# Kernel tuning notes

Measured on AMD Instinct MI355X. Metric: run time of the kernel, lower is better.

## Reference

```python
import jax, jax.numpy as jnp
import numpy as np

P_MINUS_1 = 1.0      # p=2 -> (p-1)
LCP_BETA = 32.0
LOG_ALPHA = float(np.log(2.0))  # alpha=2.0
KDIG = 8
N_HEAD = 16


def _rope(x, cos, sin):
    # x: (B,T,H,D), cos/sin: (T,D//2)
    d = x.shape[-1] // 2
    x1, x2 = x[..., :d], x[..., d:]
    c = cos[None, :, None, :]
    s = sin[None, :, None, :]
    return jnp.concatenate([x1 * c - x2 * s, x1 * s + x2 * c], axis=-1)


def _rms_norm(x, eps=1e-6):
    return x * jax.lax.rsqrt(jnp.mean(jnp.square(x), axis=-1, keepdims=True) + eps)


def setup_inputs() -> dict:
    key = jax.random.key(0)
    ks = jax.random.split(key, 9)
    B, T, C, H = 2, 512, 1024, N_HEAD
    D = C // H
    std = 0.02
    x = jax.random.normal(ks[0], (B, T, C), jnp.float32)
    cos = jax.random.uniform(ks[1], (T, D // 2), jnp.float32)
    sin = jax.random.uniform(ks[2], (T, D // 2), jnp.float32)
    Wq = jax.random.normal(ks[3], (C, C), jnp.float32) * std
    Wk = jax.random.normal(ks[4], (C, C), jnp.float32) * std
    Wv = jax.random.normal(ks[5], (C, C), jnp.float32) * std
    Wo = jax.random.normal(ks[6], (C, C), jnp.float32) * std
    # to_digits_* use flax default lecun_normal: std = 1/sqrt(fan_in)
    Wdq = jax.random.normal(ks[7], (D, KDIG), jnp.float32) / np.sqrt(D)
    Wdk = jax.random.normal(ks[8], (D, KDIG), jnp.float32) / np.sqrt(D)
    return {"x": x, "cos": cos, "sin": sin, "Wq": Wq, "Wk": Wk, "Wv": Wv,
            "Wo": Wo, "Wdq": Wdq, "Wdk": Wdk}


def _soft_lcp_depth(q_digits, k_digits):
    # q_digits: (B,H,Tq,K), k_digits: (B,H,Tk,K) -> (B,H,Tq,Tk)
    diff = jnp.abs(q_digits[:, :, :, None, :] - k_digits[:, :, None, :, :])
    match_prob = jnp.exp(-LCP_BETA * jnp.square(diff))
    prefix_prob = jnp.cumprod(match_prob, axis=-1)
    return jnp.sum(prefix_prob, axis=-1)


def reference(x, cos, sin, Wq, Wk, Wv, Wo, Wdq, Wdk):
    B, T, C = x.shape
    H = N_HEAD
    D = C // H
    q = (x @ Wq).reshape(B, T, H, D)
    k = (x @ Wk).reshape(B, T, H, D)
    v = (x @ Wv).reshape(B, T, H, D)
    q = _rms_norm(_rope(q, cos, sin))
    k = _rms_norm(_rope(k, cos, sin))
    q = jnp.transpose(q, (0, 2, 1, 3))  # (B,H,T,D)
    k = jnp.transpose(k, (0, 2, 1, 3))
    v = jnp.transpose(v, (0, 2, 1, 3))
    # causal keep mask (T,T), broadcast over (B,H)
    keep = jnp.tril(jnp.ones((T, T), dtype=bool))[None, None]
    q_digits = jax.nn.sigmoid((q @ Wdq).astype(jnp.float32)) * P_MINUS_1
    k_digits = jax.nn.sigmoid((k @ Wdk).astype(jnp.float32)) * P_MINUS_1
    lcp = _soft_lcp_depth(q_digits, k_digits)  # (B,H,T,T)
    weights = jnp.exp(lcp * LOG_ALPHA)
    weights = jnp.where(keep, weights, 0.0)
    denom = jnp.maximum(jnp.sum(weights, axis=-1, keepdims=True), 1e-9)
    attn = weights / denom
    y = jnp.einsum('bhqk,bhkd->bhqd', attn.astype(v.dtype), v)
    y = jnp.transpose(y, (0, 2, 1, 3)).reshape(B, T, C)
    return y @ Wo
```

## Files before the change

### kernel.cpp

```cpp
#include <hip/hip_runtime.h>

#define T_SEQ 512
#define CDIM  1024
#define NH    16
#define DH    64
#define BB    2
#define KD    8

#define BETA_LOG2E 46.16624131f
#define LOG2E      1.4426950408889634f

typedef unsigned short u16;
typedef __attribute__((ext_vector_type(8))) short bf16x8;
typedef __attribute__((ext_vector_type(4))) float f32x4;

__device__ inline u16 f2bf(float f) {
    unsigned int u = __builtin_bit_cast(unsigned int, f);
    unsigned int r = (u + 0x7fffu + ((u >> 16) & 1u)) >> 16;
    return (u16)r;
}
__device__ inline float bf2f(u16 v) {
    unsigned int u = ((unsigned int)v) << 16;
    return __builtin_bit_cast(float, u);
}

__device__ inline void gload_lds16(const void* g, void* l) {
    __builtin_amdgcn_global_load_lds(
        (const __attribute__((address_space(1))) void*)g,
        (__attribute__((address_space(3))) void*)l, 16, 0, 0);
}

#define PIPE_BAR_VM4()  do { asm volatile("s_waitcnt vmcnt(4)\n\ts_barrier" ::: "memory"); __builtin_amdgcn_sched_barrier(0); } while (0)
#define PIPE_BAR_VM3()  do { asm volatile("s_waitcnt vmcnt(3)\n\ts_barrier" ::: "memory"); __builtin_amdgcn_sched_barrier(0); } while (0)
#define PIPE_BAR_VM0()  do { asm volatile("s_waitcnt vmcnt(0)\n\ts_barrier" ::: "memory"); __builtin_amdgcn_sched_barrier(0); } while (0)
#define PIPE_BAR_END()  do { asm volatile("s_waitcnt lgkmcnt(0)\n\ts_barrier" ::: "memory"); __builtin_amdgcn_sched_barrier(0); } while (0)

__global__ __launch_bounds__(256)
void prep_kernel(const float* __restrict__ x,
                 const float* __restrict__ W0, const float* __restrict__ W1,
                 const float* __restrict__ W2, const float* __restrict__ W3,
                 u16* __restrict__ xb,
                 u16* __restrict__ T0, u16* __restrict__ T1,
                 u16* __restrict__ T2, u16* __restrict__ T3)
{
    const int tid = threadIdx.x;
    if (blockIdx.z == 4) {
        const int row = blockIdx.y * 32 + (tid >> 3);
        const int col = blockIdx.x * 32 + (tid & 7) * 4;
        float4 v = *(const float4*)&x[(size_t)row * CDIM + col];
        ushort4 o = { f2bf(v.x), f2bf(v.y), f2bf(v.z), f2bf(v.w) };
        *(ushort4*)&xb[(size_t)row * CDIM + col] = o;
        return;
    }
    __shared__ u16 tile[32][33];
    const float* W = (blockIdx.z == 0) ? W0 : (blockIdx.z == 1) ? W1
                   : (blockIdx.z == 2) ? W2 : W3;
    u16* Tt        = (blockIdx.z == 0) ? T0 : (blockIdx.z == 1) ? T1
                   : (blockIdx.z == 2) ? T2 : T3;
    const int k0 = blockIdx.y * 32, n0 = blockIdx.x * 32;
    const int r = tid >> 3, c4 = (tid & 7) * 4;

    float4 v = *(const float4*)&W[(size_t)(k0 + r) * CDIM + n0 + c4];
    tile[r][c4 + 0] = f2bf(v.x);
    tile[r][c4 + 1] = f2bf(v.y);
    tile[r][c4 + 2] = f2bf(v.z);
    tile[r][c4 + 3] = f2bf(v.w);
    __syncthreads();
    ushort4 o;
    o.x = tile[c4 + 0][r];
    o.y = tile[c4 + 1][r];
    o.z = tile[c4 + 2][r];
    o.w = tile[c4 + 3][r];
    *(ushort4*)&Tt[(size_t)(n0 + r) * CDIM + k0 + c4] = o;
}

__global__ __launch_bounds__(256)
void gemm_qkv_fused(const u16* __restrict__ A,
                    const u16* __restrict__ Bq, const u16* __restrict__ Bk,
                    const u16* __restrict__ Bv,
                    const float* __restrict__ cosp, const float* __restrict__ sinp,
                    const float* __restrict__ Wdq, const float* __restrict__ Wdk,
                    float* __restrict__ qdig, float* __restrict__ kdig,
                    u16* __restrict__ Vt)
{
    __shared__ __align__(16) char smem[32768];
    u16* As = (u16*)smem;
    u16* Bs = As + 8192;
    float* Cf = (float*)smem;

    const int wg = (blockIdx.x & 7) * 96 + (blockIdx.x >> 3);
    const int z = wg >> 8;
    const int rem = wg & 255;
    const int h = rem & 15;
    const int m0 = (rem >> 4) * 64;
    const int n0 = h * 64;

    const u16* Bt = (z == 0) ? Bq : (z == 1) ? Bk : Bv;

    const int tid = threadIdx.x;
    const int l = tid & 63, w = tid >> 6;
    const int wr = (w >> 1) * 32, wc = (w & 1) * 32;
    const int srow = l >> 3;
    const int sslot = (l & 7) ^ srow;

    f32x4 acc[2][2];
    #pragma unroll
    for (int i = 0; i < 2; ++i)
        #pragma unroll
        for (int j = 0; j < 2; ++j)
            acc[i][j] = (f32x4){0.f, 0.f, 0.f, 0.f};

    auto STAGE = [&](int buf, int k0) {
        #pragma unroll
        for (int q = 0; q < 2; ++q) {
            const int row = w * 16 + q * 8 + srow;
            gload_lds16(A  + (size_t)(m0 + row) * CDIM + k0 + sslot * 8,
                        &As[buf * 4096 + (w * 16 + q * 8) * 64]);
            gload_lds16(Bt + (size_t)(n0 + row) * CDIM + k0 + sslot * 8,
                        &Bs[buf * 4096 + (w * 16 + q * 8) * 64]);
        }
    };

    STAGE(0, 0);
    for (int t = 0; t < 16; ++t) {
        const int cur = t & 1;
        if (t < 15) {
            STAGE(cur ^ 1, (t + 1) * 64);
            PIPE_BAR_VM4();
        } else {
            PIPE_BAR_VM0();
        }

        const u16* Ab = &As[cur * 4096];
        const u16* Bb = &Bs[cur * 4096];
        bf16x8 af[2][2], bfr[2][2];
        #pragma unroll
        for (int i = 0; i < 2; ++i)
            #pragma unroll
            for (int kh = 0; kh < 2; ++kh) {
                const int ra = wr + i * 16 + (l & 15);
                const int sa = (kh * 4 + (l >> 4)) ^ (ra & 7);
                af[i][kh] = *(const bf16x8*)&Ab[ra * 64 + sa * 8];
                const int rb = wc + i * 16 + (l & 15);
                const int sb = (kh * 4 + (l >> 4)) ^ (rb & 7);
                bfr[i][kh] = *(const bf16x8*)&Bb[rb * 64 + sb * 8];
            }
        #pragma unroll
        for (int kh = 0; kh < 2; ++kh)
            #pragma unroll
            for (int i = 0; i < 2; ++i)
                #pragma unroll
                for (int j = 0; j < 2; ++j)
                    acc[i][j] = __builtin_amdgcn_mfma_f32_16x16x32_bf16(
                        af[i][kh], bfr[j][kh], acc[i][j], 0, 0, 0);
        PIPE_BAR_END();
    }
    __syncthreads();

    if (z == 2) {
        #pragma unroll
        for (int i = 0; i < 2; ++i)
            #pragma unroll
            for (int j = 0; j < 2; ++j) {
                const int mm = wr + i * 16 + (l >> 4) * 4;
                const int dd = wc + j * 16 + (l & 15);
                #pragma unroll
                for (int r = 0; r < 4; ++r)
                    Cf[dd * 65 + mm + r] = acc[i][j][r];
            }
        __syncthreads();
        const int b = m0 >> 9, t0 = m0 & (T_SEQ - 1);
        u16* vbase = Vt + ((size_t)(b * NH + h) * 64) * T_SEQ;
        #pragma unroll
        for (int it = 0; it < 16; ++it) {
            const int d = it * 4 + w;
            vbase[(size_t)d * T_SEQ + t0 + l] = f2bf(Cf[d * 65 + l]);
        }
        return;
    }

    #pragma unroll
    for (int i = 0; i < 2; ++i)
        #pragma unroll
        for (int j = 0; j < 2; ++j) {
            const int mm = wr + i * 16 + (l >> 4) * 4;
            const int dd = wc + j * 16 + (l & 15);
            #pragma unroll
            for (int r = 0; r < 4; ++r)
                Cf[(mm + r) * 65 + dd] = acc[i][j][r];
        }

    const float* Wd = z ? Wdk : Wdq;
    float* dig = z ? kdig : qdig;

    const int dl = l & 15, rq = l >> 4;
    float wreg[4][8];
    #pragma unroll
    for (int d4 = 0; d4 < 4; ++d4) {
        *(float4*)&wreg[d4][0] = *(const float4*)&Wd[(dl + d4 * 16) * 8];
        *(float4*)&wreg[d4][4] = *(const float4*)&Wd[(dl + d4 * 16) * 8 + 4];
    }
    __syncthreads();

    for (int g = 0; g < 4; ++g) {
        const int m = w * 16 + g * 4 + rq;
        const int mg = m0 + m;
        const int b = mg >> 9, t = mg & (T_SEQ - 1);

        const float* cr = &Cf[m * 65];
        float r0 = cr[dl], r1 = cr[dl + 16], r2 = cr[dl + 32], r3 = cr[dl + 48];
        float c0 = cosp[t * 32 + dl], c1 = cosp[t * 32 + dl + 16];
        float s0 = sinp[t * 32 + dl], s1 = sinp[t * 32 + dl + 16];
        float v0 = r0 * c0 - r2 * s0;
        float v1 = r1 * c1 - r3 * s1;
        float v2 = r0 * s0 + r2 * c0;
        float v3 = r1 * s1 + r3 * c1;

        float ss = v0 * v0 + v1 * v1 + v2 * v2 + v3 * v3;
        #pragma unroll
        for (int off = 1; off < 16; off <<= 1) ss += __shfl_xor(ss, off);
        float sc = rsqrtf(ss * (1.0f / 64.0f) + 1e-6f);
        v0 *= sc; v1 *= sc; v2 *= sc; v3 *= sc;

        float zz[8];
        #pragma unroll
        for (int j = 0; j < 8; ++j)
            zz[j] = v0 * wreg[0][j] + v1 * wreg[1][j] + v2 * wreg[2][j] + v3 * wreg[3][j];
        #pragma unroll
        for (int j = 0; j < 8; ++j) {
            #pragma unroll
            for (int off = 1; off < 16; off <<= 1) zz[j] += __shfl_xor(zz[j], off);
        }
        float zsel = zz[0];
        #pragma unroll
        for (int j = 1; j < 8; ++j) zsel = (dl == j) ? zz[j] : zsel;
        if (dl < 8)
            dig[((size_t)(b * NH + h) * T_SEQ + t) * KD + dl] =
                1.0f / (1.0f + exp2f(-LOG2E * zsel));
    }
}

__global__ __launch_bounds__(256)
void attn_partial(const float* __restrict__ qdig, const float* __restrict__ kdig,
                  const u16* __restrict__ Vt,
                  u16* __restrict__ pacc, float* __restrict__ pdeng)
{
    __shared__ u16 Vs[4096];
    __shared__ u16 Ps[4096];
    __shared__ float qds[512];

    const int tid = threadIdx.x;
    const int w = tid >> 6, l = tid & 63;

    const int wg = (blockIdx.x & 7) * 144 + (blockIdx.x >> 3);
    const int tile = wg % 36;
    const int bh = wg / 36;
    const size_t bhT = (size_t)bh * T_SEQ;

    int id = tile, c = 0;
    while (id >= c + 1) { id -= (c + 1); ++c; }
    const int kt = id;
    const int k0 = kt * 64;

    const int srow = l >> 3, sslot = (l & 7) ^ srow;
    #pragma unroll
    for (int q2 = 0; q2 < 2; ++q2) {
        const int R0 = w * 16 + q2 * 8;
        gload_lds16(Vt + ((size_t)bh * 64 + R0 + srow) * T_SEQ + k0 + sslot * 8,
                    &Vs[R0 * 64]);
    }
    *(float2*)&qds[tid * 2] = *(const float2*)&qdig[(bhT + c * 64) * KD + tid * 2];

    float kd[8];
    {
        const float* kp = &kdig[(bhT + k0 + l) * KD];
        *(float4*)&kd[0] = *(const float4*)kp;
        *(float4*)&kd[4] = *(const float4*)(kp + 4);
    }
    __syncthreads();

    const bool diag = (kt == c);
    for (int qi = 0; qi < 16; ++qi) {
        const int qrow = w * 16 + qi;
        float qd[8];
        *(float4*)&qd[0] = *(const float4*)&qds[qrow * 8];
        *(float4*)&qd[4] = *(const float4*)&qds[qrow * 8 + 4];
        float S = 0.f, lcp = 0.f;
        #pragma unroll
        for (int jj = 0; jj < 8; ++jj) {
            float d = qd[jj] - kd[jj];
            S += d * d;
            lcp += exp2f(-BETA_LOG2E * S);
        }
        float wgt = exp2f(lcp);
        if (diag && l > qrow) wgt = 0.f;
        Ps[qrow * 64 + (((l >> 3) ^ (qi & 7)) << 3) + (l & 7)] = f2bf(wgt);
    }
    __syncthreads();

    const int wr = (w >> 1) * 32, wc = (w & 1) * 32;
    f32x4 acc[2][2], accd[2];
    #pragma unroll
    for (int i = 0; i < 2; ++i) {
        accd[i] = (f32x4){0.f, 0.f, 0.f, 0.f};
        #pragma unroll
        for (int j = 0; j < 2; ++j) acc[i][j] = (f32x4){0.f, 0.f, 0.f, 0.f};
    }
    bf16x8 ones;
    #pragma unroll
    for (int i = 0; i < 8; ++i) ones[i] = (short)0x3F80;

    #pragma unroll
    for (int kh = 0; kh < 2; ++kh) {
        bf16x8 af[2], bfr[2];
        #pragma unroll
        for (int i = 0; i < 2; ++i) {
            const int ra = wr + i * 16 + (l & 15);
            const int sa = (kh * 4 + (l >> 4)) ^ (ra & 7);
            af[i] = *(const bf16x8*)&Ps[ra * 64 + sa * 8];
            const int rb = wc + i * 16 + (l & 15);
            const int sb = (kh * 4 + (l >> 4)) ^ (rb & 7);
            bfr[i] = *(const bf16x8*)&Vs[rb * 64 + sb * 8];
        }
        #pragma unroll
        for (int i = 0; i < 2; ++i) {
            accd[i] = __builtin_amdgcn_mfma_f32_16x16x32_bf16(af[i], ones, accd[i], 0, 0, 0);
            #pragma unroll
            for (int j = 0; j < 2; ++j)
                acc[i][j] = __builtin_amdgcn_mfma_f32_16x16x32_bf16(
                    af[i], bfr[j], acc[i][j], 0, 0, 0);
        }
    }

    const int task = bh * 36 + tile;
    u16* pa = pacc + (size_t)task * 4096;
    #pragma unroll
    for (int i = 0; i < 2; ++i) {
        const int row = wr + i * 16 + (l >> 4) * 4;
        #pragma unroll
        for (int j = 0; j < 2; ++j) {
            const int col = wc + j * 16 + (l & 15);
            #pragma unroll
            for (int r = 0; r < 4; ++r)
                pa[(size_t)(row + r) * 64 + col] = f2bf(acc[i][j][r]);
        }
        if ((l & 15) == 0) {
            #pragma unroll
            for (int r = 0; r < 4; ++r)
                pdeng[(size_t)task * 64 + row + r] = accd[i][r];
        }
    }
}

__global__ __launch_bounds__(256)
void attn_combine(const u16* __restrict__ pacc, const float* __restrict__ pdeng,
                  u16* __restrict__ y)
{
    const int c = blockIdx.x >> 1, half = blockIdx.x & 1;
    const int h = blockIdx.y, b = blockIdx.z;
    const int tid = threadIdx.x;
    const int r = tid >> 2, cg = (tid & 3) * 8 + half * 32;
    const int base = (b * NH + h) * 36 + c * (c + 1) / 2;

    float acc[8] = {};
    float den = 0.f;
    for (int kt = 0; kt <= c; ++kt) {
        const u16* pa = pacc + (size_t)(base + kt) * 4096 + r * 64 + cg;
        ushort4 v0 = *(const ushort4*)(pa + 0);
        ushort4 v1 = *(const ushort4*)(pa + 4);
        acc[0] += bf2f(v0.x); acc[1] += bf2f(v0.y);
        acc[2] += bf2f(v0.z); acc[3] += bf2f(v0.w);
        acc[4] += bf2f(v1.x); acc[5] += bf2f(v1.y);
        acc[6] += bf2f(v1.z); acc[7] += bf2f(v1.w);
        den += pdeng[(size_t)(base + kt) * 64 + r];
    }
    float inv = 1.f / fmaxf(den, 1e-9f);

    u16* yr = y + ((size_t)(b * T_SEQ + c * 64 + r)) * CDIM + h * DH + cg;
    uint4 p;
    p.x = f2bf(acc[0] * inv) | ((unsigned)f2bf(acc[1] * inv) << 16);
    p.y = f2bf(acc[2] * inv) | ((unsigned)f2bf(acc[3] * inv) << 16);
    p.z = f2bf(acc[4] * inv) | ((unsigned)f2bf(acc[5] * inv) << 16);
    p.w = f2bf(acc[6] * inv) | ((unsigned)f2bf(acc[7] * inv) << 16);
    *(uint4*)yr = p;
}

__global__ __launch_bounds__(256)
void gemm_proj(const u16* __restrict__ A, const u16* __restrict__ Bt,
               float* __restrict__ C)
{
    __shared__ __align__(16) u16 S[12288];

    const int wg = (blockIdx.x & 7) * 64 + (blockIdx.x >> 3);
    const int n0 = (wg & 15) * 64;
    const int m0 = (wg >> 4) * 32;

    const int tid = threadIdx.x;
    const int l = tid & 63, w = tid >> 6;
    const int wr = (w & 1) * 16, wc = (w >> 1) * 32;
    const int srow = l >> 3;
    const int sslot = (l & 7) ^ srow;

    f32x4 acc[2];
    acc[0] = (f32x4){0.f, 0.f, 0.f, 0.f};
    acc[1] = (f32x4){0.f, 0.f, 0.f, 0.f};

    auto STAGE = [&](int buf, int k0) {
        const int rowa = w * 8 + srow;
        gload_lds16(A + (size_t)(m0 + rowa) * CDIM + k0 + sslot * 8,
                    &S[buf * 2048 + (w * 8) * 64]);
        #pragma unroll
        for (int q = 0; q < 2; ++q) {
            const int row = w * 16 + q * 8 + srow;
            gload_lds16(Bt + (size_t)(n0 + row) * CDIM + k0 + sslot * 8,
                        &S[4096 + buf * 4096 + (w * 16 + q * 8) * 64]);
        }
    };

    STAGE(0, 0);
    for (int t = 0; t < 16; ++t) {
        const int cur = t & 1;
        if (t < 15) {
            STAGE(cur ^ 1, (t + 1) * 64);
            PIPE_BAR_VM3();
        } else {
            PIPE_BAR_VM0();
        }

        const u16* Ab = &S[cur * 2048];
        const u16* Bb = &S[4096 + cur * 4096];
        #pragma unroll
        for (int kh = 0; kh < 2; ++kh) {
            const int ra = wr + (l & 15);
            const int sa = (kh * 4 + (l >> 4)) ^ (ra & 7);
            bf16x8 af = *(const bf16x8*)&Ab[ra * 64 + sa * 8];
            #pragma unroll
            for (int j = 0; j < 2; ++j) {
                const int rb = wc + j * 16 + (l & 15);
                const int sb = (kh * 4 + (l >> 4)) ^ (rb & 7);
                bf16x8 bfr = *(const bf16x8*)&Bb[rb * 64 + sb * 8];
                acc[j] = __builtin_amdgcn_mfma_f32_16x16x32_bf16(
                    af, bfr, acc[j], 0, 0, 0);
            }
        }
        PIPE_BAR_END();
    }

    #pragma unroll
    for (int j = 0; j < 2; ++j) {
        const int row = m0 + wr + (l >> 4) * 4;
        const int col = n0 + wc + j * 16 + (l & 15);
        #pragma unroll
        for (int r = 0; r < 4; ++r)
            C[(size_t)(row + r) * CDIM + col] = acc[j][r];
    }
}

extern "C" void kernel_launch(void* const* d_in, const int* in_sizes, int n_in,
                              void* d_out, int out_size, void* d_ws, size_t ws_size,
                              hipStream_t stream)
{
    (void)in_sizes; (void)n_in; (void)out_size; (void)ws_size;
    const float* x    = (const float*)d_in[0];
    const float* cosp = (const float*)d_in[1];
    const float* sinp = (const float*)d_in[2];
    const float* Wq   = (const float*)d_in[3];
    const float* Wk   = (const float*)d_in[4];
    const float* Wv   = (const float*)d_in[5];
    const float* Wo   = (const float*)d_in[6];
    const float* Wdq  = (const float*)d_in[7];
    const float* Wdk  = (const float*)d_in[8];
    float* out = (float*)d_out;

    const int M = BB * T_SEQ;
    const size_t MC = (size_t)M * CDIM;
    char* p = (char*)d_ws;
    float* qdig = (float*)p; p += (size_t)M * NH * KD * 4;
    float* kdig = (float*)p; p += (size_t)M * NH * KD * 4;
    u16* xb   = (u16*)p; p += MC * 2;
    u16* wqt  = (u16*)p; p += MC * 2;
    u16* wkt  = (u16*)p; p += MC * 2;
    u16* wvt  = (u16*)p; p += MC * 2;
    u16* wot  = (u16*)p; p += MC * 2;
    u16* Vt   = (u16*)p; p += MC * 2;
    u16* ybuf = (u16*)p; p += MC * 2;
    u16* pacc = (u16*)p; p += (size_t)1152 * 4096 * 2;
    float* pdeng = (float*)p; p += (size_t)1152 * 64 * 4;

    dim3 blk(256);
    prep_kernel<<<dim3(32, 32, 5), blk, 0, stream>>>(
        x, Wq, Wk, Wv, Wo, xb, wqt, wkt, wvt, wot);
    gemm_qkv_fused<<<dim3(768), blk, 0, stream>>>(
        xb, wqt, wkt, wvt, cosp, sinp, Wdq, Wdk, qdig, kdig, Vt);
    attn_partial<<<dim3(1152), blk, 0, stream>>>(
        qdig, kdig, Vt, pacc, pdeng);
    attn_combine<<<dim3(16, NH, BB), blk, 0, stream>>>(pacc, pdeng, ybuf);
    gemm_proj<<<dim3(512), blk, 0, stream>>>(ybuf, wot, out);
}
```

Baseline: 58.27 us.

## Fuse attention partial combine into output projection GEMM A-tile load

Removes the separate attn_combine kernel and the ybuf round trip: gemm_proj now sums the per-key-tile partial outputs and denominators while staging its A tile in LDS, then normalizes and converts to bf16. attn_partial now stages its partial accumulator through LDS so global writes become coalesced 16-byte stores. This saves a kernel launch and an intermediate write/read. In exchange, the partial reduction is repeated by every column-tile block, and the GEMM drops its double-buffered async prefetch pipeline for synchronous per-step loads.

```diff
diff --git a/kernel.cpp b/kernel.cpp
--- a/kernel.cpp
+++ b/kernel.cpp
@@ -23,6 +23,10 @@
     unsigned int u = ((unsigned int)v) << 16;
     return __builtin_bit_cast(float, u);
 }
+__device__ inline void add2(float* a, unsigned v) {
+    a[0] += bf2f((u16)(v & 0xffffu));
+    a[1] += bf2f((u16)(v >> 16));
+}
 
 __device__ inline void gload_lds16(const void* g, void* l) {
     __builtin_amdgcn_global_load_lds(
@@ -31,7 +35,6 @@
 }
 
 #define PIPE_BAR_VM4()  do { asm volatile("s_waitcnt vmcnt(4)\n\ts_barrier" ::: "memory"); __builtin_amdgcn_sched_barrier(0); } while (0)
-#define PIPE_BAR_VM3()  do { asm volatile("s_waitcnt vmcnt(3)\n\ts_barrier" ::: "memory"); __builtin_amdgcn_sched_barrier(0); } while (0)
 #define PIPE_BAR_VM0()  do { asm volatile("s_waitcnt vmcnt(0)\n\ts_barrier" ::: "memory"); __builtin_amdgcn_sched_barrier(0); } while (0)
 #define PIPE_BAR_END()  do { asm volatile("s_waitcnt lgkmcnt(0)\n\ts_barrier" ::: "memory"); __builtin_amdgcn_sched_barrier(0); } while (0)
 
@@ -333,7 +336,8 @@
     }
 
     const int task = bh * 36 + tile;
-    u16* pa = pacc + (size_t)task * 4096;
+
+    __syncthreads();
     #pragma unroll
     for (int i = 0; i < 2; ++i) {
         const int row = wr + i * 16 + (l >> 4) * 4;
@@ -342,7 +346,7 @@
             const int col = wc + j * 16 + (l & 15);
             #pragma unroll
             for (int r = 0; r < 4; ++r)
-                pa[(size_t)(row + r) * 64 + col] = f2bf(acc[i][j][r]);
+                Ps[(row + r) * 64 + col] = f2bf(acc[i][j][r]);
         }
         if ((l & 15) == 0) {
             #pragma unroll
@@ -350,100 +354,105 @@
                 pdeng[(size_t)task * 64 + row + r] = accd[i][r];
         }
     }
+    __syncthreads();
+    {
+        const int row = tid >> 2;
+        const int seg = (tid & 3) * 16;
+        uint4* dst = (uint4*)(pacc + (size_t)task * 4096 + row * 64 + seg);
+        const uint4* src = (const uint4*)&Ps[row * 64 + seg];
+        dst[0] = src[0];
+        dst[1] = src[1];
+    }
 }
 
 __global__ __launch_bounds__(256)
-void attn_combine(const u16* __restrict__ pacc, const float* __restrict__ pdeng,
-                  u16* __restrict__ y)
+void gemm_proj(const u16* __restrict__ pacc, const float* __restrict__ pdeng,
+               const u16* __restrict__ Bt, float* __restrict__ C)
 {
-    const int c = blockIdx.x >> 1, half = blockIdx.x & 1;
-    const int h = blockIdx.y, b = blockIdx.z;
-    const int tid = threadIdx.x;
-    const int r = tid >> 2, cg = (tid & 3) * 8 + half * 32;
-    const int base = (b * NH + h) * 36 + c * (c + 1) / 2;
-
-    float acc[8] = {};
-    float den = 0.f;
-    for (int kt = 0; kt <= c; ++kt) {
-        const u16* pa = pacc + (size_t)(base + kt) * 4096 + r * 64 + cg;
-        ushort4 v0 = *(const ushort4*)(pa + 0);
-        ushort4 v1 = *(const ushort4*)(pa + 4);
-        acc[0] += bf2f(v0.x); acc[1] += bf2f(v0.y);
-        acc[2] += bf2f(v0.z); acc[3] += bf2f(v0.w);
-        acc[4] += bf2f(v1.x); acc[5] += bf2f(v1.y);
-        acc[6] += bf2f(v1.z); acc[7] += bf2f(v1.w);
-        den += pdeng[(size_t)(base + kt) * 64 + r];
-    }
-    float inv = 1.f / fmaxf(den, 1e-9f);
-
-    u16* yr = y + ((size_t)(b * T_SEQ + c * 64 + r)) * CDIM + h * DH + cg;
-    uint4 p;
-    p.x = f2bf(acc[0] * inv) | ((unsigned)f2bf(acc[1] * inv) << 16);
-    p.y = f2bf(acc[2] * inv) | ((unsigned)f2bf(acc[3] * inv) << 16);
-    p.z = f2bf(acc[4] * inv) | ((unsigned)f2bf(acc[5] * inv) << 16);
-    p.w = f2bf(acc[6] * inv) | ((unsigned)f2bf(acc[7] * inv) << 16);
-    *(uint4*)yr = p;
-}
-
-__global__ __launch_bounds__(256)
-void gemm_proj(const u16* __restrict__ A, const u16* __restrict__ Bt,
-               float* __restrict__ C)
-{
-    __shared__ __align__(16) u16 S[12288];
+    __shared__ __align__(16) u16 As[32 * 128];
+    __shared__ __align__(16) u16 Bs[64 * 128];
+    __shared__ float invs[NH * 32];
 
     const int wg = (blockIdx.x & 7) * 64 + (blockIdx.x >> 3);
     const int n0 = (wg & 15) * 64;
     const int m0 = (wg >> 4) * 32;
+    const int b = m0 >> 9;
+    const int c = (m0 & 511) >> 6;
+    const int rbase = m0 & 32;
+    const int cbase = c * (c + 1) / 2;
 
     const int tid = threadIdx.x;
     const int l = tid & 63, w = tid >> 6;
     const int wr = (w & 1) * 16, wc = (w >> 1) * 32;
-    const int srow = l >> 3;
-    const int sslot = (l & 7) ^ srow;
+
+    {
+        const int r = tid & 31;
+        #pragma unroll
+        for (int hh = 0; hh < 2; ++hh) {
+            const int h = (tid >> 5) + hh * 8;
+            const int base = (b * NH + h) * 36 + cbase;
+            float den = 0.f;
+            for (int kt = 0; kt <= c; ++kt)
+                den += pdeng[(size_t)(base + kt) * 64 + rbase + r];
+            invs[h * 32 + r] = 1.f / fmaxf(den, 1e-9f);
+        }
+    }
 
     f32x4 acc[2];
     acc[0] = (f32x4){0.f, 0.f, 0.f, 0.f};
     acc[1] = (f32x4){0.f, 0.f, 0.f, 0.f};
 
-    auto STAGE = [&](int buf, int k0) {
-        const int rowa = w * 8 + srow;
-        gload_lds16(A + (size_t)(m0 + rowa) * CDIM + k0 + sslot * 8,
-                    &S[buf * 2048 + (w * 8) * 64]);
-        #pragma unroll
-        for (int q = 0; q < 2; ++q) {
-            const int row = w * 16 + q * 8 + srow;
-            gload_lds16(Bt + (size_t)(n0 + row) * CDIM + k0 + sslot * 8,
-                        &S[4096 + buf * 4096 + (w * 16 + q * 8) * 64]);
-        }
-    };
-
-    STAGE(0, 0);
-    for (int t = 0; t < 16; ++t) {
-        const int cur = t & 1;
-        if (t < 15) {
-            STAGE(cur ^ 1, (t + 1) * 64);
-            PIPE_BAR_VM3();
-        } else {
-            PIPE_BAR_VM0();
-        }
-
-        const u16* Ab = &S[cur * 2048];
-        const u16* Bb = &S[4096 + cur * 4096];
-        #pragma unroll
-        for (int kh = 0; kh < 2; ++kh) {
+    const int arow = tid >> 3;
+    const int adg  = (tid & 7) * 8;
+
+    for (int t = 0; t < 8; ++t) {
+        __syncthreads();
+
+        #pragma unroll
+        for (int hh = 0; hh < 2; ++hh) {
+            const int h = t * 2 + hh;
+            const int base = (b * NH + h) * 36 + cbase;
+            float a8[8] = {};
+            for (int kt = 0; kt <= c; ++kt) {
+                const u16* ps = pacc + (size_t)(base + kt) * 4096
+                              + (rbase + arow) * 64 + adg;
+                uint4 v = *(const uint4*)ps;
+                add2(&a8[0], v.x); add2(&a8[2], v.y);
+                add2(&a8[4], v.z); add2(&a8[6], v.w);
+            }
+            const float inv = invs[h * 32 + arow];
+            uint4 o;
+            o.x = f2bf(a8[0] * inv) | ((unsigned)f2bf(a8[1] * inv) << 16);
+            o.y = f2bf(a8[2] * inv) | ((unsigned)f2bf(a8[3] * inv) << 16);
+            o.z = f2bf(a8[4] * inv) | ((unsigned)f2bf(a8[5] * inv) << 16);
+            o.w = f2bf(a8[6] * inv) | ((unsigned)f2bf(a8[7] * inv) << 16);
+            const int slot = (hh * 8 + (adg >> 3)) ^ (arow & 15);
+            *(uint4*)&As[arow * 128 + slot * 8] = o;
+        }
+
+        #pragma unroll
+        for (int q = 0; q < 4; ++q) {
+            const int row = w * 16 + q * 4 + (l >> 4);
+            const int slot = (l & 15) ^ (row & 15);
+            gload_lds16(Bt + (size_t)(n0 + row) * CDIM + t * 128 + slot * 8,
+                        &Bs[(w * 16 + q * 4) * 128]);
+        }
+        __syncthreads();
+
+        #pragma unroll
+        for (int kh = 0; kh < 4; ++kh) {
             const int ra = wr + (l & 15);
-            const int sa = (kh * 4 + (l >> 4)) ^ (ra & 7);
-            bf16x8 af = *(const bf16x8*)&Ab[ra * 64 + sa * 8];
+            const int sa = (kh * 4 + (l >> 4)) ^ (ra & 15);
+            bf16x8 af = *(const bf16x8*)&As[ra * 128 + sa * 8];
             #pragma unroll
             for (int j = 0; j < 2; ++j) {
                 const int rb = wc + j * 16 + (l & 15);
-                const int sb = (kh * 4 + (l >> 4)) ^ (rb & 7);
-                bf16x8 bfr = *(const bf16x8*)&Bb[rb * 64 + sb * 8];
+                const int sb = (kh * 4 + (l >> 4)) ^ (rb & 15);
+                bf16x8 bfr = *(const bf16x8*)&Bs[rb * 128 + sb * 8];
                 acc[j] = __builtin_amdgcn_mfma_f32_16x16x32_bf16(
                     af, bfr, acc[j], 0, 0, 0);
             }
         }
-        PIPE_BAR_END();
     }
 
     #pragma unroll
@@ -483,7 +492,6 @@
     u16* wvt  = (u16*)p; p += MC * 2;
     u16* wot  = (u16*)p; p += MC * 2;
     u16* Vt   = (u16*)p; p += MC * 2;
-    u16* ybuf = (u16*)p; p += MC * 2;
     u16* pacc = (u16*)p; p += (size_t)1152 * 4096 * 2;
     float* pdeng = (float*)p; p += (size_t)1152 * 64 * 4;
 
@@ -494,6 +502,5 @@
         xb, wqt, wkt, wvt, cosp, sinp, Wdq, Wdk, qdig, kdig, Vt);
     attn_partial<<<dim3(1152), blk, 0, stream>>>(
         qdig, kdig, Vt, pacc, pdeng);
-    attn_combine<<<dim3(16, NH, BB), blk, 0, stream>>>(pacc, pdeng, ybuf);
-    gemm_proj<<<dim3(512), blk, 0, stream>>>(ybuf, wot, out);
-}
+    gemm_proj<<<dim3(512), blk, 0, stream>>>(pacc, pdeng, wot, out);
+}
```

Result: slower. 89.54 us (+53.7%).

## Fuse all stages into one cooperative persistent kernel with grid syncs

Applied to the files above, without the earlier changes.

Turns the five kernels into device task functions and runs them from a single cooperative persistent kernel that loops over tasks and separates stages with grid.sync(). The aim is to remove per-kernel launch overhead and inter-kernel gaps. The cost is that the grid is capped by occupancy (up to 768 blocks), so stages with more tasks run in several rounds. Shared memory is unified at 32KB, which may lower occupancy for the lighter stages. If the cooperative launch fails, the original multi-kernel path runs instead.

```diff
diff --git a/kernel.cpp b/kernel.cpp
--- a/kernel.cpp
+++ b/kernel.cpp
@@ -1,4 +1,7 @@
 #include <hip/hip_runtime.h>
+#include <hip/hip_cooperative_groups.h>
+
+namespace cg = cooperative_groups;
 
 #define T_SEQ 512
 #define CDIM  1024
@@ -35,31 +38,33 @@
 #define PIPE_BAR_VM0()  do { asm volatile("s_waitcnt vmcnt(0)\n\ts_barrier" ::: "memory"); __builtin_amdgcn_sched_barrier(0); } while (0)
 #define PIPE_BAR_END()  do { asm volatile("s_waitcnt lgkmcnt(0)\n\ts_barrier" ::: "memory"); __builtin_amdgcn_sched_barrier(0); } while (0)
 
-__global__ __launch_bounds__(256)
-void prep_kernel(const float* __restrict__ x,
-                 const float* __restrict__ W0, const float* __restrict__ W1,
-                 const float* __restrict__ W2, const float* __restrict__ W3,
-                 u16* __restrict__ xb,
-                 u16* __restrict__ T0, u16* __restrict__ T1,
-                 u16* __restrict__ T2, u16* __restrict__ T3)
+
+__device__ void prep_task(int task, char* SMEM,
+                          const float* x,
+                          const float* W0, const float* W1,
+                          const float* W2, const float* W3,
+                          u16* xb, u16* T0, u16* T1, u16* T2, u16* T3)
 {
     const int tid = threadIdx.x;
-    if (blockIdx.z == 4) {
-        const int row = blockIdx.y * 32 + (tid >> 3);
-        const int col = blockIdx.x * 32 + (tid & 7) * 4;
+    const int z = task >> 10;
+    const int rem = task & 1023;
+    const int bx = rem & 31, by = rem >> 5;
+
+    if (z == 4) {
+        const int row = by * 32 + (tid >> 3);
+        const int col = bx * 32 + (tid & 7) * 4;
         float4 v = *(const float4*)&x[(size_t)row * CDIM + col];
         ushort4 o = { f2bf(v.x), f2bf(v.y), f2bf(v.z), f2bf(v.w) };
         *(ushort4*)&xb[(size_t)row * CDIM + col] = o;
         return;
     }
-    __shared__ u16 tile[32][33];
-    const float* W = (blockIdx.z == 0) ? W0 : (blockIdx.z == 1) ? W1
-                   : (blockIdx.z == 2) ? W2 : W3;
-    u16* Tt        = (blockIdx.z == 0) ? T0 : (blockIdx.z == 1) ? T1
-                   : (blockIdx.z == 2) ? T2 : T3;
-    const int k0 = blockIdx.y * 32, n0 = blockIdx.x * 32;
+    u16 (*tile)[33] = (u16(*)[33])SMEM;
+    const float* W = (z == 0) ? W0 : (z == 1) ? W1 : (z == 2) ? W2 : W3;
+    u16* Tt        = (z == 0) ? T0 : (z == 1) ? T1 : (z == 2) ? T2 : T3;
+    const int k0 = by * 32, n0 = bx * 32;
     const int r = tid >> 3, c4 = (tid & 7) * 4;
 
+    __syncthreads();
     float4 v = *(const float4*)&W[(size_t)(k0 + r) * CDIM + n0 + c4];
     tile[r][c4 + 0] = f2bf(v.x);
     tile[r][c4 + 1] = f2bf(v.y);
@@ -74,21 +79,18 @@
     *(ushort4*)&Tt[(size_t)(n0 + r) * CDIM + k0 + c4] = o;
 }
 
-__global__ __launch_bounds__(256)
-void gemm_qkv_fused(const u16* __restrict__ A,
-                    const u16* __restrict__ Bq, const u16* __restrict__ Bk,
-                    const u16* __restrict__ Bv,
-                    const float* __restrict__ cosp, const float* __restrict__ sinp,
-                    const float* __restrict__ Wdq, const float* __restrict__ Wdk,
-                    float* __restrict__ qdig, float* __restrict__ kdig,
-                    u16* __restrict__ Vt)
-{
-    __shared__ __align__(16) char smem[32768];
-    u16* As = (u16*)smem;
+__device__ void qkv_task(int task, char* SMEM,
+                         const u16* A, const u16* Bq, const u16* Bk,
+                         const u16* Bv,
+                         const float* cosp, const float* sinp,
+                         const float* Wdq, const float* Wdk,
+                         float* qdig, float* kdig, u16* Vt)
+{
+    u16* As = (u16*)SMEM;
     u16* Bs = As + 8192;
-    float* Cf = (float*)smem;
-
-    const int wg = (blockIdx.x & 7) * 96 + (blockIdx.x >> 3);
+    float* Cf = (float*)SMEM;
+
+    const int wg = (task & 7) * 96 + (task >> 3);
     const int z = wg >> 8;
     const int rem = wg & 255;
     const int h = rem & 15;
@@ -121,6 +123,7 @@
         }
     };
 
+    __syncthreads();
     STAGE(0, 0);
     for (int t = 0; t < 16; ++t) {
         const int cur = t & 1;
@@ -240,19 +243,18 @@
     }
 }
 
-__global__ __launch_bounds__(256)
-void attn_partial(const float* __restrict__ qdig, const float* __restrict__ kdig,
-                  const u16* __restrict__ Vt,
-                  u16* __restrict__ pacc, float* __restrict__ pdeng)
-{
-    __shared__ u16 Vs[4096];
-    __shared__ u16 Ps[4096];
-    __shared__ float qds[512];
+__device__ void partial_task(int task, char* SMEM,
+                             const float* qdig, const float* kdig,
+                             const u16* Vt, u16* pacc, float* pdeng)
+{
+    u16* Vs = (u16*)SMEM;
+    u16* Ps = Vs + 4096;
+    float* qds = (float*)(SMEM + 16384);
 
     const int tid = threadIdx.x;
     const int w = tid >> 6, l = tid & 63;
 
-    const int wg = (blockIdx.x & 7) * 144 + (blockIdx.x >> 3);
+    const int wg = (task & 7) * 144 + (task >> 3);
     const int tile = wg % 36;
     const int bh = wg / 36;
     const size_t bhT = (size_t)bh * T_SEQ;
@@ -261,6 +263,8 @@
     while (id >= c + 1) { id -= (c + 1); ++c; }
     const int kt = id;
     const int k0 = kt * 64;
+
+    __syncthreads();
 
     const int srow = l >> 3, sslot = (l & 7) ^ srow;
     #pragma unroll
@@ -332,8 +336,8 @@
         }
     }
 
-    const int task = bh * 36 + tile;
-    u16* pa = pacc + (size_t)task * 4096;
+    const int task36 = bh * 36 + tile;
+    u16* pa = pacc + (size_t)task36 * 4096;
     #pragma unroll
     for (int i = 0; i < 2; ++i) {
         const int row = wr + i * 16 + (l >> 4) * 4;
@@ -347,25 +351,26 @@
         if ((l & 15) == 0) {
             #pragma unroll
             for (int r = 0; r < 4; ++r)
-                pdeng[(size_t)task * 64 + row + r] = accd[i][r];
-        }
-    }
-}
-
-__global__ __launch_bounds__(256)
-void attn_combine(const u16* __restrict__ pacc, const float* __restrict__ pdeng,
-                  u16* __restrict__ y)
-{
-    const int c = blockIdx.x >> 1, half = blockIdx.x & 1;
-    const int h = blockIdx.y, b = blockIdx.z;
+                pdeng[(size_t)task36 * 64 + row + r] = accd[i][r];
+        }
+    }
+}
+
+__device__ void combine_task(int task,
+                             const u16* pacc, const float* pdeng, u16* y)
+{
+    const int xg = task & 15;
+    const int h = (task >> 4) & 15;
+    const int b = task >> 8;
+    const int c = xg >> 1, half = xg & 1;
     const int tid = threadIdx.x;
-    const int r = tid >> 2, cg = (tid & 3) * 8 + half * 32;
+    const int r = tid >> 2, cg2 = (tid & 3) * 8 + half * 32;
     const int base = (b * NH + h) * 36 + c * (c + 1) / 2;
 
     float acc[8] = {};
     float den = 0.f;
     for (int kt = 0; kt <= c; ++kt) {
-        const u16* pa = pacc + (size_t)(base + kt) * 4096 + r * 64 + cg;
+        const u16* pa = pacc + (size_t)(base + kt) * 4096 + r * 64 + cg2;
         ushort4 v0 = *(const ushort4*)(pa + 0);
         ushort4 v1 = *(const ushort4*)(pa + 4);
         acc[0] += bf2f(v0.x); acc[1] += bf2f(v0.y);
@@ -376,7 +381,7 @@
     }
     float inv = 1.f / fmaxf(den, 1e-9f);
 
-    u16* yr = y + ((size_t)(b * T_SEQ + c * 64 + r)) * CDIM + h * DH + cg;
+    u16* yr = y + ((size_t)(b * T_SEQ + c * 64 + r)) * CDIM + h * DH + cg2;
     uint4 p;
     p.x = f2bf(acc[0] * inv) | ((unsigned)f2bf(acc[1] * inv) << 16);
     p.y = f2bf(acc[2] * inv) | ((unsigned)f2bf(acc[3] * inv) << 16);
@@ -385,13 +390,12 @@
     *(uint4*)yr = p;
 }
 
-__global__ __launch_bounds__(256)
-void gemm_proj(const u16* __restrict__ A, const u16* __restrict__ Bt,
-               float* __restrict__ C)
-{
-    __shared__ __align__(16) u16 S[12288];
-
-    const int wg = (blockIdx.x & 7) * 64 + (blockIdx.x >> 3);
+__device__ void proj_task(int task, char* SMEM,
+                          const u16* A, const u16* Bt, float* C)
+{
+    u16* S = (u16*)SMEM;
+
+    const int wg = (task & 7) * 64 + (task >> 3);
     const int n0 = (wg & 15) * 64;
     const int m0 = (wg >> 4) * 32;
 
@@ -417,6 +421,7 @@
         }
     };
 
+    __syncthreads();
     STAGE(0, 0);
     for (int t = 0; t < 16; ++t) {
         const int cur = t & 1;
@@ -454,6 +459,82 @@
         for (int r = 0; r < 4; ++r)
             C[(size_t)(row + r) * CDIM + col] = acc[j][r];
     }
+}
+
+__global__ __launch_bounds__(256, 2)
+void ultrametric_mega(const float* x, const float* cosp, const float* sinp,
+                      const float* Wq, const float* Wk, const float* Wv,
+                      const float* Wo, const float* Wdq, const float* Wdk,
+                      u16* xb, u16* wqt, u16* wkt, u16* wvt, u16* wot,
+                      float* qdig, float* kdig, u16* Vt, u16* ybuf,
+                      u16* pacc, float* pdeng, float* out)
+{
+    __shared__ __align__(16) char SMEM[32768];
+    cg::grid_group grid = cg::this_grid();
+    const int stride = gridDim.x;
+
+    for (int task = blockIdx.x; task < 5120; task += stride)
+        prep_task(task, SMEM, x, Wq, Wk, Wv, Wo, xb, wqt, wkt, wvt, wot);
+    grid.sync();
+
+    for (int task = blockIdx.x; task < 768; task += stride)
+        qkv_task(task, SMEM, xb, wqt, wkt, wvt, cosp, sinp, Wdq, Wdk,
+                 qdig, kdig, Vt);
+    grid.sync();
+
+    for (int task = blockIdx.x; task < 1152; task += stride)
+        partial_task(task, SMEM, qdig, kdig, Vt, pacc, pdeng);
+    grid.sync();
+
+    for (int task = blockIdx.x; task < 512; task += stride)
+        combine_task(task, pacc, pdeng, ybuf);
+    grid.sync();
+
+    for (int task = blockIdx.x; task < 512; task += stride)
+        proj_task(task, SMEM, ybuf, wot, out);
+}
+
+__global__ __launch_bounds__(256)
+void prep_kernel(const float* x, const float* W0, const float* W1,
+                 const float* W2, const float* W3,
+                 u16* xb, u16* T0, u16* T1, u16* T2, u16* T3)
+{
+    __shared__ __align__(16) char SMEM[2176];
+    prep_task(blockIdx.z * 1024 + blockIdx.y * 32 + blockIdx.x, SMEM,
+              x, W0, W1, W2, W3, xb, T0, T1, T2, T3);
+}
+
+__global__ __launch_bounds__(256)
+void qkv_kernel(const u16* A, const u16* Bq, const u16* Bk, const u16* Bv,
+                const float* cosp, const float* sinp,
+                const float* Wdq, const float* Wdk,
+                float* qdig, float* kdig, u16* Vt)
+{
+    __shared__ __align__(16) char SMEM[32768];
+    qkv_task(blockIdx.x, SMEM, A, Bq, Bk, Bv, cosp, sinp, Wdq, Wdk,
+             qdig, kdig, Vt);
+}
+
+__global__ __launch_bounds__(256)
+void partial_kernel(const float* qdig, const float* kdig, const u16* Vt,
+                    u16* pacc, float* pdeng)
+{
+    __shared__ __align__(16) char SMEM[18432];
+    partial_task(blockIdx.x, SMEM, qdig, kdig, Vt, pacc, pdeng);
+}
+
+__global__ __launch_bounds__(256)
+void combine_kernel(const u16* pacc, const float* pdeng, u16* y)
+{
+    combine_task(blockIdx.z * 256 + blockIdx.y * 16 + blockIdx.x,
+                 pacc, pdeng, y);
+}
+
+__global__ __launch_bounds__(256)
+void proj_kernel(const u16* A, const u16* Bt, float* C)
+{
+    __shared__ __align__(16) char SMEM[24576];
+    proj_task(blockIdx.x, SMEM, A, Bt, C);
 }
 
 extern "C" void kernel_launch(void* const* d_in, const int* in_sizes, int n_in,
@@ -487,13 +568,37 @@
     u16* pacc = (u16*)p; p += (size_t)1152 * 4096 * 2;
     float* pdeng = (float*)p; p += (size_t)1152 * 64 * 4;
 
+    bool coop_ok = false;
+    {
+        int maxPerCU = 0;
+        hipError_t qerr = hipOccupancyMaxActiveBlocksPerMultiprocessor(
+            &maxPerCU, (const void*)ultrametric_mega, 256, 0);
+        long cap = (qerr == hipSuccess) ? (long)maxPerCU * 256 : 0;
+        int grid = (int)(cap < 768 ? cap : 768);
+        if (grid >= 256) {
+            void* kargs[] = {
+                (void*)&x, (void*)&cosp, (void*)&sinp,
+                (void*)&Wq, (void*)&Wk, (void*)&Wv, (void*)&Wo,
+                (void*)&Wdq, (void*)&Wdk,
+                (void*)&xb, (void*)&wqt, (void*)&wkt, (void*)&wvt, (void*)&wot,
+                (void*)&qdig, (void*)&kdig, (void*)&Vt, (void*)&ybuf,
+                (void*)&pacc, (void*)&pdeng, (void*)&out
+            };
+            hipError_t lerr = hipLaunchCooperativeKernel(
+                (const void*)ultrametric_mega, dim3(grid), dim3(256),
+                kargs, 0, stream);
+            coop_ok = (lerr == hipSuccess);
+        }
+    }
+    if (coop_ok) return;
+
     dim3 blk(256);
     prep_kernel<<<dim3(32, 32, 5), blk, 0, stream>>>(
         x, Wq, Wk, Wv, Wo, xb, wqt, wkt, wvt, wot);
-    gemm_qkv_fused<<<dim3(768), blk, 0, stream>>>(
+    qkv_kernel<<<dim3(768), blk, 0, stream>>>(
         xb, wqt, wkt, wvt, cosp, sinp, Wdq, Wdk, qdig, kdig, Vt);
-    attn_partial<<<dim3(1152), blk, 0, stream>>>(
+    partial_kernel<<<dim3(1152), blk, 0, stream>>>(
         qdig, kdig, Vt, pacc, pdeng);
-    attn_combine<<<dim3(16, NH, BB), blk, 0, stream>>>(pacc, pdeng, ybuf);
-    gemm_proj<<<dim3(512), blk, 0, stream>>>(ybuf, wot, out);
-}
+    combine_kernel<<<dim3(16, NH, BB), blk, 0, stream>>>(pacc, pdeng, ybuf);
+    proj_kernel<<<dim3(512), blk, 0, stream>>>(ybuf, wot, out);
+}
```

Result: slower. 208.3 us (+257.4%).
